# Performance work log

Hardware: AMD Instinct MI355X
Metric: run time of the kernel (lower is better)

## Reference

```python
import jax, jax.numpy as jnp
import numpy as np

B, HD, NQ, NC, NH, NL, NP, NLAY, DFF = 8, 256, 300, 80, 8, 3, 4, 6, 1024
SHAPES = [(80, 80), (40, 40), (20, 20)]
FEAT_CH = [512, 1024, 2048]
DH = HD // NH
EPS_ANCHOR = 0.01


def _linear(x, w, b):
    return x @ w.T + b


def _ln(x, g, b):
    m = x.mean(-1, keepdims=True)
    v = ((x - m) ** 2).mean(-1, keepdims=True)
    return (x - m) / jnp.sqrt(v + 1e-5) * g + b


def _mlp3(x, w1, b1, w2, b2, w3, b3):
    x = jax.nn.relu(_linear(x, w1, b1))
    x = jax.nn.relu(_linear(x, w2, b2))
    return _linear(x, w3, b3)


def _inv_sigmoid(x, eps=1e-5):
    x = jnp.clip(x, 0.0, 1.0)
    return jnp.log(jnp.clip(x, eps, None) / jnp.clip(1.0 - x, eps, None))


def _anchors():
    parts = []
    for lvl, (h, w) in enumerate(SHAPES):
        gy, gx = jnp.meshgrid(jnp.arange(h, dtype=jnp.float32), jnp.arange(w, dtype=jnp.float32), indexing='ij')
        xy = jnp.stack([(gx + 0.5) / w, (gy + 0.5) / h], -1).reshape(-1, 2)
        wh = jnp.full_like(xy, 0.05 * (2.0 ** lvl))
        parts.append(jnp.concatenate([xy, wh], -1))
    a = jnp.concatenate(parts, 0)[None]  # [1, L, 4]
    valid = jnp.all((a > EPS_ANCHOR) & (a < 1 - EPS_ANCHOR), -1, keepdims=True)
    a = jnp.log(a / (1 - a))
    a = jnp.where(valid, a, jnp.float32(1e6))  # finite sentinel for torch's inf
    return a, valid.astype(jnp.float32)


def _mha(q_in, k_in, v_in, wqkv, bqkv, wo, bo):
    wq, wk, wv = jnp.split(wqkv, 3, 0)
    bq, bk, bv = jnp.split(bqkv, 3, 0)
    q = _linear(q_in, wq, bq)
    k = _linear(k_in, wk, bk)
    v = _linear(v_in, wv, bv)
    Bq = q.shape[0]
    sp = lambda t: t.reshape(Bq, -1, NH, DH).transpose(0, 2, 1, 3)
    q, k, v = sp(q), sp(k), sp(v)
    att = jax.nn.softmax(jnp.einsum('bhqd,bhkd->bhqk', q, k) * (1.0 / np.sqrt(DH)), -1)
    out = jnp.einsum('bhqk,bhkd->bhqd', att, v).transpose(0, 2, 1, 3).reshape(Bq, -1, HD)
    return _linear(out, wo, bo)


def _msda(value, loc, aw):
    # value [B,Len,NH,DH], loc [B,Q,NH,NL,NP,2] in [0,1], aw [B,Q,NH,NL,NP]
    Bq, Q = loc.shape[0], loc.shape[1]
    out = jnp.zeros((Bq, Q, NH, DH), value.dtype)
    start = 0
    for lvl, (h, w) in enumerate(SHAPES):
        v = value[:, start:start + h * w]  # [B,hw,NH,DH]
        start += h * w
        # grid_sample align_corners=False pixel coords
        x = loc[..., lvl, :, 0] * w - 0.5  # [B,Q,NH,NP]
        y = loc[..., lvl, :, 1] * h - 0.5
        x0 = jnp.floor(x)
        y0 = jnp.floor(y)
        lx = x - x0
        ly = y - y0
        acc = jnp.zeros((Bq, Q, NH, NP, DH), value.dtype)
        for dy, dx, wt in ((0, 0, (1 - lx) * (1 - ly)), (0, 1, lx * (1 - ly)), (1, 0, (1 - lx) * ly), (1, 1, lx * ly)):
            xi = x0 + dx
            yi = y0 + dy
            ok = ((xi >= 0) & (xi < w) & (yi >= 0) & (yi < h)).astype(value.dtype)  # zero padding
            idx = (jnp.clip(yi, 0, h - 1) * w + jnp.clip(xi, 0, w - 1)).astype(jnp.int32)
            idxf = idx.transpose(0, 1, 3, 2).reshape(Bq, Q * NP, NH)
            g = jnp.take_along_axis(v, idxf[..., None], axis=1)  # [B,Q*NP,NH,DH]
            g = g.reshape(Bq, Q, NP, NH, DH).transpose(0, 1, 3, 2, 4)
            acc = acc + g * (wt * ok)[..., None]
        out = out + (acc * aw[..., lvl, :, None]).sum(3)
    return out.reshape(Bq, Q, HD)


def reference(feat0, feat1, feat2, pw0, bg0, bb0, pw1, bg1, bb1, pw2, bg2, bb2,
              eo_w, eo_b, eln_g, eln_b, es_w, es_b,
              eb_w1, eb_b1, eb_w2, eb_b2, eb_w3, eb_b3,
              qp_w1, qp_b1, qp_w2, qp_b2,
              d_qkv_w, d_qkv_b, d_ao_w, d_ao_b, d_ln1_g, d_ln1_b,
              d_off_w, d_off_b, d_aw_w, d_aw_b, d_val_w, d_val_b,
              d_out_w, d_out_b, d_ln2_g, d_ln2_b,
              d_f1_w, d_f1_b, d_f2_w, d_f2_b, d_ln3_g, d_ln3_b,
              d_sc_w, d_sc_b, d_bb_w1, d_bb_b1, d_bb_w2, d_bb_b2, d_bb_w3, d_bb_b3):
    feats = [feat0, feat1, feat2]
    pws, bgs, bbs = [pw0, pw1, pw2], [bg0, bg1, bg2], [bb0, bb1, bb2]
    toks = []
    for f, pw, g, b in zip(feats, pws, bgs, bbs):
        # 1x1 conv (no bias) + BatchNorm eval (running mean 0, var 1 -> affine)
        t = jnp.einsum('bchw,oc->bhwo', f, pw) * g + b
        toks.append(t.reshape(f.shape[0], -1, HD))
    memory = jnp.concatenate(toks, 1)  # [B, 8400, 256]
    anchors, valid = _anchors()
    memory = memory * valid
    out_mem = _ln(_linear(memory, eo_w, eo_b), eln_g, eln_b)
    scores = _linear(out_mem, es_w, es_b)  # [B,L,NC]
    _, topi = jax.lax.top_k(scores.max(-1), NQ)  # 'default' query select
    gather = lambda t: jnp.take_along_axis(t, topi[..., None], axis=1)
    sel_mem = gather(out_mem)
    anc_b = jnp.broadcast_to(anchors, (memory.shape[0],) + anchors.shape[1:])
    ref_unact = _mlp3(sel_mem, eb_w1, eb_b1, eb_w2, eb_b2, eb_w3, eb_b3) + gather(anc_b)
    tgt = jax.lax.stop_gradient(sel_mem)
    ref = jax.nn.sigmoid(jax.lax.stop_gradient(ref_unact))  # [B,NQ,4]
    Bq = memory.shape[0]
    for i in range(NLAY):
        qpos = _linear(jax.nn.relu(_linear(ref, qp_w1, qp_b1)), qp_w2, qp_b2)
        q = tgt + qpos
        a = _mha(q, q, tgt, d_qkv_w[i], d_qkv_b[i], d_ao_w[i], d_ao_b[i])
        tgt = _ln(tgt + a, d_ln1_g[i], d_ln1_b[i])
        qc = tgt + qpos
        off = _linear(qc, d_off_w[i], d_off_b[i]).reshape(Bq, NQ, NH, NL, NP, 2)
        aw = jax.nn.softmax(_linear(qc, d_aw_w[i], d_aw_b[i]).reshape(Bq, NQ, NH, NL * NP), -1)
        aw = aw.reshape(Bq, NQ, NH, NL, NP)
        r = ref[:, :, None, None, None, :]
        loc = r[..., :2] + off / NP * r[..., 2:] * 0.5
        val = _linear(memory, d_val_w[i], d_val_b[i]).reshape(Bq, -1, NH, DH)
        ca = _linear(_msda(val, loc, aw), d_out_w[i], d_out_b[i])
        tgt = _ln(tgt + ca, d_ln2_g[i], d_ln2_b[i])
        f = _linear(jax.nn.relu(_linear(tgt, d_f1_w[i], d_f1_b[i])), d_f2_w[i], d_f2_b[i])
        tgt = _ln(tgt + f, d_ln3_g[i], d_ln3_b[i])
        delta = _mlp3(tgt, d_bb_w1[i], d_bb_b1[i], d_bb_w2[i], d_bb_b2[i], d_bb_w3[i], d_bb_b3[i])
        new_ref = jax.nn.sigmoid(delta + _inv_sigmoid(ref))
        ref = jax.lax.stop_gradient(new_ref) if i < NLAY - 1 else new_ref
    logits = _linear(tgt, d_sc_w[-1], d_sc_b[-1])
    return jnp.concatenate([logits, ref], -1)  # [B, NQ, NC+4]


def setup_inputs():
    key = jax.random.key(0)
    ks = iter(jax.random.split(key, 80))
    def rn(shape, s=0.02):
        return jax.random.normal(next(ks), shape, jnp.float32) * s
    inp = {}
    for i, (c, (h, w)) in enumerate(zip(FEAT_CH, SHAPES)):
        inp['feat%d' % i] = rn((B, c, h, w), 1.0)
        inp['pw%d' % i] = rn((HD, c), (2.0 / c) ** 0.5)
        inp['bg%d' % i] = jnp.ones((HD,), jnp.float32)
        inp['bb%d' % i] = jnp.zeros((HD,), jnp.float32)
    inp['eo_w'] = rn((HD, HD)); inp['eo_b'] = jnp.zeros((HD,), jnp.float32)
    inp['eln_g'] = jnp.ones((HD,), jnp.float32); inp['eln_b'] = jnp.zeros((HD,), jnp.float32)
    inp['es_w'] = rn((NC, HD)); inp['es_b'] = jnp.zeros((NC,), jnp.float32)
    inp['eb_w1'] = rn((HD, HD)); inp['eb_b1'] = jnp.zeros((HD,), jnp.float32)
    inp['eb_w2'] = rn((HD, HD)); inp['eb_b2'] = jnp.zeros((HD,), jnp.float32)
    inp['eb_w3'] = rn((4, HD)); inp['eb_b3'] = jnp.zeros((4,), jnp.float32)
    inp['qp_w1'] = rn((2 * HD, 4)); inp['qp_b1'] = jnp.zeros((2 * HD,), jnp.float32)
    inp['qp_w2'] = rn((HD, 2 * HD)); inp['qp_b2'] = jnp.zeros((HD,), jnp.float32)
    L = NLAY
    inp['d_qkv_w'] = rn((L, 3 * HD, HD)); inp['d_qkv_b'] = jnp.zeros((L, 3 * HD), jnp.float32)
    inp['d_ao_w'] = rn((L, HD, HD)); inp['d_ao_b'] = jnp.zeros((L, HD), jnp.float32)
    inp['d_ln1_g'] = jnp.ones((L, HD), jnp.float32); inp['d_ln1_b'] = jnp.zeros((L, HD), jnp.float32)
    inp['d_off_w'] = rn((L, NH * NL * NP * 2, HD), 0.005); inp['d_off_b'] = rn((L, NH * NL * NP * 2), 0.1)
    inp['d_aw_w'] = rn((L, NH * NL * NP, HD)); inp['d_aw_b'] = jnp.zeros((L, NH * NL * NP), jnp.float32)
    inp['d_val_w'] = rn((L, HD, HD)); inp['d_val_b'] = jnp.zeros((L, HD), jnp.float32)
    inp['d_out_w'] = rn((L, HD, HD)); inp['d_out_b'] = jnp.zeros((L, HD), jnp.float32)
    inp['d_ln2_g'] = jnp.ones((L, HD), jnp.float32); inp['d_ln2_b'] = jnp.zeros((L, HD), jnp.float32)
    inp['d_f1_w'] = rn((L, DFF, HD)); inp['d_f1_b'] = jnp.zeros((L, DFF), jnp.float32)
    inp['d_f2_w'] = rn((L, HD, DFF)); inp['d_f2_b'] = jnp.zeros((L, HD), jnp.float32)
    inp['d_ln3_g'] = jnp.ones((L, HD), jnp.float32); inp['d_ln3_b'] = jnp.zeros((L, HD), jnp.float32)
    inp['d_sc_w'] = rn((L, NC, HD)); inp['d_sc_b'] = jnp.zeros((L, NC), jnp.float32)
    inp['d_bb_w1'] = rn((L, HD, HD)); inp['d_bb_b1'] = jnp.zeros((L, HD), jnp.float32)
    inp['d_bb_w2'] = rn((L, HD, HD)); inp['d_bb_b2'] = jnp.zeros((L, HD), jnp.float32)
    inp['d_bb_w3'] = rn((L, 4, HD)); inp['d_bb_b3'] = jnp.zeros((L, 4), jnp.float32)
    return inp
```

## Files before the change

kernel.cpp:

```cpp
#include <hip/hip_runtime.h>

constexpr int Bb  = 8;
constexpr int HDn = 256;
constexpr int NQn = 300;
constexpr int NCn = 80;
constexpr int NHn = 8;
constexpr int NPn = 4;
constexpr int Sn  = 8400;
constexpr int MQ  = Bb * NQn;
constexpr int MS  = Bb * Sn;

typedef __attribute__((ext_vector_type(8))) short short8;
typedef __attribute__((ext_vector_type(4))) float floatx4;

__device__ __forceinline__ unsigned short f2bf(float f) {
    unsigned u = __float_as_uint(f);
    unsigned r = u + 0x7FFFu + ((u >> 16) & 1u);
    return (unsigned short)(r >> 16);
}
__device__ __forceinline__ unsigned pack2(float a, float b) {
    return (unsigned)f2bf(a) | ((unsigned)f2bf(b) << 16);
}

__global__ __launch_bounds__(256) void proj_kernel(
    const float* __restrict__ feat, const float* __restrict__ pw,
    const float* __restrict__ bg, const float* __restrict__ bb,
    float* __restrict__ mem,
    int C, int HW, int Wdim, int base)
{
    const int b = blockIdx.z;
    const float* Afeat = feat + (size_t)b * C * HW;
    __shared__ float As[16][128];
    __shared__ float Ws[16][64];
    const int tid = threadIdx.x;
    const int tx = tid & 15, ty = tid >> 4;
    const int p0 = blockIdx.x * 128, o0 = blockIdx.y * 64;
    const int pp4 = (tid & 31) * 4;
    const int cb = tid >> 5;
    const int wrow = tid & 63, wk = (tid >> 6) * 4;
    float acc[8][4] = {};
    for (int k0 = 0; k0 < C; k0 += 16) {
        float4 va0 = make_float4(0.f,0.f,0.f,0.f), va1 = va0;
        if (p0 + pp4 < HW) {
            va0 = *reinterpret_cast<const float4*>(Afeat + (size_t)(k0 + cb) * HW + p0 + pp4);
            va1 = *reinterpret_cast<const float4*>(Afeat + (size_t)(k0 + cb + 8) * HW + p0 + pp4);
        }
        const float4 vw = *reinterpret_cast<const float4*>(pw + (size_t)(o0 + wrow) * C + k0 + wk);
        __syncthreads();
        As[cb][pp4 + 0] = va0.x; As[cb][pp4 + 1] = va0.y; As[cb][pp4 + 2] = va0.z; As[cb][pp4 + 3] = va0.w;
        As[cb + 8][pp4 + 0] = va1.x; As[cb + 8][pp4 + 1] = va1.y; As[cb + 8][pp4 + 2] = va1.z; As[cb + 8][pp4 + 3] = va1.w;
        Ws[wk + 0][wrow] = vw.x; Ws[wk + 1][wrow] = vw.y; Ws[wk + 2][wrow] = vw.z; Ws[wk + 3][wrow] = vw.w;
        __syncthreads();
#pragma unroll
        for (int k = 0; k < 16; ++k) {
            const float4 a0 = *reinterpret_cast<const float4*>(&As[k][ty * 8]);
            const float4 a1 = *reinterpret_cast<const float4*>(&As[k][ty * 8 + 4]);
            const float4 w4 = *reinterpret_cast<const float4*>(&Ws[k][tx * 4]);
            const float av[8] = {a0.x, a0.y, a0.z, a0.w, a1.x, a1.y, a1.z, a1.w};
            const float wv[4] = {w4.x, w4.y, w4.z, w4.w};
#pragma unroll
            for (int i = 0; i < 8; ++i)
#pragma unroll
                for (int j = 0; j < 4; ++j)
                    acc[i][j] = fmaf(av[i], wv[j], acc[i][j]);
        }
    }
#pragma unroll
    for (int i = 0; i < 8; ++i) {
        const int pp = p0 + ty * 8 + i;
        if (pp >= HW) continue;
        const int yy = pp / Wdim, xx = pp - yy * Wdim;
        const float ax = (xx + 0.5f) / Wdim, ay = (yy + 0.5f) / Wdim;
        const float vm = ((ax > 0.01f) && (ax < 0.99f) && (ay > 0.01f) && (ay < 0.99f)) ? 1.f : 0.f;
#pragma unroll
        for (int j = 0; j < 4; ++j) {
            const int o = o0 + tx * 4 + j;
            mem[((size_t)b * Sn + base + pp) * HDn + o] = (acc[i][j] * bg[o] + bb[o]) * vm;
        }
    }
}

__global__ __launch_bounds__(512) void gemm_eoln(
    const float* __restrict__ A,
    const float* __restrict__ W,
    const float* __restrict__ bias,
    const float* __restrict__ g, const float* __restrict__ bt,
    float* __restrict__ O)
{
    __shared__ float As[16][128];
    __shared__ float Ws[16][256];
    const int tid = threadIdx.x;
    const int tx = tid & 31;
    const int ty = tid >> 5;
    const int m0 = blockIdx.x * 128;
    const int arow = tid >> 2, ak = (tid & 3) * 4;
    const int wrow = tid >> 1, wk = (tid & 1) * 8;
    float acc[8][8] = {};
    for (int k0 = 0; k0 < 256; k0 += 16) {
        const float4 a4 = *reinterpret_cast<const float4*>(A + (size_t)(m0 + arow) * 256 + k0 + ak);
        const float4 w0 = *reinterpret_cast<const float4*>(W + (size_t)wrow * 256 + k0 + wk);
        const float4 w1 = *reinterpret_cast<const float4*>(W + (size_t)wrow * 256 + k0 + wk + 4);
        __syncthreads();
        As[ak + 0][arow] = a4.x; As[ak + 1][arow] = a4.y; As[ak + 2][arow] = a4.z; As[ak + 3][arow] = a4.w;
        Ws[wk + 0][wrow] = w0.x; Ws[wk + 1][wrow] = w0.y; Ws[wk + 2][wrow] = w0.z; Ws[wk + 3][wrow] = w0.w;
        Ws[wk + 4][wrow] = w1.x; Ws[wk + 5][wrow] = w1.y; Ws[wk + 6][wrow] = w1.z; Ws[wk + 7][wrow] = w1.w;
        __syncthreads();
#pragma unroll
        for (int k = 0; k < 16; ++k) {
            const float4 a0 = *reinterpret_cast<const float4*>(&As[k][ty * 8]);
            const float4 a1 = *reinterpret_cast<const float4*>(&As[k][ty * 8 + 4]);
            const float4 wv0 = *reinterpret_cast<const float4*>(&Ws[k][tx * 8]);
            const float4 wv1 = *reinterpret_cast<const float4*>(&Ws[k][tx * 8 + 4]);
            const float av[8] = {a0.x, a0.y, a0.z, a0.w, a1.x, a1.y, a1.z, a1.w};
            const float wv[8] = {wv0.x, wv0.y, wv0.z, wv0.w, wv1.x, wv1.y, wv1.z, wv1.w};
#pragma unroll
            for (int i = 0; i < 8; ++i)
#pragma unroll
                for (int j = 0; j < 8; ++j)
                    acc[i][j] = fmaf(av[i], wv[j], acc[i][j]);
        }
    }
    float bv[8], gv[8], btv[8];
#pragma unroll
    for (int j = 0; j < 8; ++j) {
        bv[j] = bias[tx * 8 + j];
        gv[j] = g[tx * 8 + j];
        btv[j] = bt[tx * 8 + j];
    }
#pragma unroll
    for (int i = 0; i < 8; ++i) {
        float s1 = 0.f, s2 = 0.f;
#pragma unroll
        for (int j = 0; j < 8; ++j) {
            const float v = acc[i][j] + bv[j];
            acc[i][j] = v;
            s1 += v; s2 += v * v;
        }
#pragma unroll
        for (int o = 1; o < 32; o <<= 1) {
            s1 += __shfl_xor(s1, o, 64);
            s2 += __shfl_xor(s2, o, 64);
        }
        const float mean = s1 * (1.f / 256.f);
        const float var  = s2 * (1.f / 256.f) - mean * mean;
        const float inv  = rsqrtf(var + 1e-5f);
        float out[8];
#pragma unroll
        for (int j = 0; j < 8; ++j) out[j] = (acc[i][j] - mean) * inv * gv[j] + btv[j];
        float* op = O + (size_t)(m0 + ty * 8 + i) * 256 + tx * 8;
        *reinterpret_cast<float4*>(op) = make_float4(out[0], out[1], out[2], out[3]);
        *reinterpret_cast<float4*>(op + 4) = make_float4(out[4], out[5], out[6], out[7]);
    }
}

__global__ __launch_bounds__(256) void gemm_es(
    const float* __restrict__ A,
    const float* __restrict__ W,
    const float* __restrict__ bias,
    float* __restrict__ smax)
{
    __shared__ float As[16][64];
    __shared__ float Ws[16][80];
    const int tid = threadIdx.x;
    const int tx = tid & 15;
    const int ty = tid >> 4;
    const int m0 = blockIdx.x * 64;
    const int arow = tid >> 2, ak = (tid & 3) * 4;
    float acc[4][5] = {};
    for (int k0 = 0; k0 < 256; k0 += 16) {
        const float4 a4 = *reinterpret_cast<const float4*>(A + (size_t)(m0 + arow) * 256 + k0 + ak);
        float4 w0 = make_float4(0.f,0.f,0.f,0.f), w1 = w0;
        const int wrow = tid >> 1, wk = (tid & 1) * 8;
        if (tid < 160) {
            w0 = *reinterpret_cast<const float4*>(W + (size_t)wrow * 256 + k0 + wk);
            w1 = *reinterpret_cast<const float4*>(W + (size_t)wrow * 256 + k0 + wk + 4);
        }
        __syncthreads();
        As[ak + 0][arow] = a4.x; As[ak + 1][arow] = a4.y; As[ak + 2][arow] = a4.z; As[ak + 3][arow] = a4.w;
        if (tid < 160) {
            Ws[wk + 0][wrow] = w0.x; Ws[wk + 1][wrow] = w0.y; Ws[wk + 2][wrow] = w0.z; Ws[wk + 3][wrow] = w0.w;
            Ws[wk + 4][wrow] = w1.x; Ws[wk + 5][wrow] = w1.y; Ws[wk + 6][wrow] = w1.z; Ws[wk + 7][wrow] = w1.w;
        }
        __syncthreads();
#pragma unroll
        for (int k = 0; k < 16; ++k) {
            const float4 a4v = *reinterpret_cast<const float4*>(&As[k][ty * 4]);
            const float av[4] = {a4v.x, a4v.y, a4v.z, a4v.w};
            float wv[5];
#pragma unroll
            for (int j = 0; j < 5; ++j) wv[j] = Ws[k][tx * 5 + j];
#pragma unroll
            for (int i = 0; i < 4; ++i)
#pragma unroll
                for (int j = 0; j < 5; ++j)
                    acc[i][j] = fmaf(av[i], wv[j], acc[i][j]);
        }
    }
    float bv[5];
#pragma unroll
    for (int j = 0; j < 5; ++j) bv[j] = bias[tx * 5 + j];
#pragma unroll
    for (int i = 0; i < 4; ++i) {
        float vmax = -3.0e38f;
#pragma unroll
        for (int j = 0; j < 5; ++j) vmax = fmaxf(vmax, acc[i][j] + bv[j]);
#pragma unroll
        for (int o = 1; o < 16; o <<= 1) vmax = fmaxf(vmax, __shfl_xor(vmax, o, 64));
        if (tx == 0) smax[m0 + ty * 4 + i] = vmax;
    }
}

__global__ void fconv_kernel(const float* __restrict__ in, unsigned short* __restrict__ out, int n4)
{
    const int i = blockIdx.x * 256 + threadIdx.x;
    if (i >= n4) return;
    const float4 v = reinterpret_cast<const float4*>(in)[i];
    reinterpret_cast<uint2*>(out)[i] = make_uint2(pack2(v.x, v.y), pack2(v.z, v.w));
}

__global__ __launch_bounds__(512) void gemm_vbig(
    const unsigned short* __restrict__ A,
    const float* __restrict__ W,
    const float* __restrict__ bias,
    unsigned short* __restrict__ C,
    int M)
{
    __shared__ __align__(16) unsigned short As[128 * 40];
    __shared__ __align__(16) unsigned short Bs[256 * 40];
    const int tid = threadIdx.x;
    const int lane = tid & 63, wid = tid >> 6;
    const int wm = wid >> 2, wn = wid & 3;
    const int m0 = blockIdx.x * 128, n0 = blockIdx.y * 256;
    const int arow = tid >> 2, ak = (tid & 3) * 8;
    const int brow = tid >> 1, bk = (tid & 1) * 16;
    const int fs = (lane >> 4) * 8;
    floatx4 acc[4][4];
#pragma unroll
    for (int i = 0; i < 4; ++i)
#pragma unroll
        for (int j = 0; j < 4; ++j) acc[i][j] = (floatx4){0.f, 0.f, 0.f, 0.f};

    for (int k0 = 0; k0 < 256; k0 += 32) {
        const short8 a8 = *reinterpret_cast<const short8*>(A + (size_t)(m0 + arow) * 256 + k0 + ak);
        float wv[16];
        {
            const float* wp = W + (size_t)(n0 + brow) * 256 + k0 + bk;
#pragma unroll
            for (int j = 0; j < 4; ++j) *reinterpret_cast<float4*>(&wv[4 * j]) = *reinterpret_cast<const float4*>(wp + 4 * j);
        }
        __syncthreads();
        *reinterpret_cast<short8*>(&As[arow * 40 + ak]) = a8;
        *reinterpret_cast<uint4*>(&Bs[brow * 40 + bk]) =
            make_uint4(pack2(wv[0], wv[1]), pack2(wv[2], wv[3]), pack2(wv[4], wv[5]), pack2(wv[6], wv[7]));
        *reinterpret_cast<uint4*>(&Bs[brow * 40 + bk + 8]) =
            make_uint4(pack2(wv[8], wv[9]), pack2(wv[10], wv[11]), pack2(wv[12], wv[13]), pack2(wv[14], wv[15]));
        __syncthreads();
        short8 af[4], bf[4];
#pragma unroll
        for (int mi = 0; mi < 4; ++mi)
            af[mi] = *reinterpret_cast<const short8*>(&As[(wm * 64 + mi * 16 + (lane & 15)) * 40 + fs]);
#pragma unroll
        for (int ni = 0; ni < 4; ++ni)
            bf[ni] = *reinterpret_cast<const short8*>(&Bs[(wn * 64 + ni * 16 + (lane & 15)) * 40 + fs]);
#pragma unroll
        for (int mi = 0; mi < 4; ++mi)
#pragma unroll
            for (int ni = 0; ni < 4; ++ni)
                acc[mi][ni] = __builtin_amdgcn_mfma_f32_16x16x32_bf16(af[mi], bf[ni], acc[mi][ni], 0, 0, 0);
    }
#pragma unroll
    for (int mi = 0; mi < 4; ++mi) {
        const int rowb = m0 + wm * 64 + mi * 16 + (lane >> 4) * 4;
#pragma unroll
        for (int ni = 0; ni < 4; ++ni) {
            const int col = n0 + wn * 64 + ni * 16 + (lane & 15);
            const float bv = bias[col];
#pragma unroll
            for (int r = 0; r < 4; ++r)
                C[(size_t)(rowb + r) * 1536 + col] = f2bf(acc[mi][ni][r] + bv);
        }
    }
}

template <int ACT>
__global__ __launch_bounds__(256) void gemm_sm(
    const float* __restrict__ A, const float* __restrict__ A2, int a2_nlim, int lda,
    const float* __restrict__ W, int ldw,
    const float* __restrict__ bias,
    float* __restrict__ C, int ldc,
    int M, int N, int K)
{
    constexpr int LD = 264;
    __shared__ __align__(16) unsigned short As[64 * LD];
    __shared__ __align__(16) unsigned short Bs[64 * LD];
    const int tid = threadIdx.x;
    const int lane = tid & 63, wid = tid >> 6;
    const int wr = wid >> 1, wc = wid & 1;
    const int m0 = blockIdx.x * 64, n0 = blockIdx.y * 64;
    const float* A2e = (A2 && n0 < a2_nlim) ? A2 : nullptr;
    const int srow = tid >> 2;
    const int cb   = (tid & 3) * 16;
    const int fs = (lane >> 4) * 8;
    floatx4 acc[2][2];
#pragma unroll
    for (int i = 0; i < 2; ++i)
#pragma unroll
        for (int j = 0; j < 2; ++j) acc[i][j] = (floatx4){0.f, 0.f, 0.f, 0.f};

    for (int kc = 0; kc < K; kc += 256) {
        if (kc) __syncthreads();
        {
            const bool mok = (m0 + srow < M);
            const float* ap = A + (size_t)(m0 + srow) * lda + kc;
            const float* ap2 = A2e ? A2e + (size_t)(m0 + srow) * lda + kc : nullptr;
#pragma unroll
            for (int c = 0; c < 4; ++c) {
                float4 v[4];
#pragma unroll
                for (int j = 0; j < 4; ++j) {
                    v[j] = make_float4(0.f, 0.f, 0.f, 0.f);
                    if (mok) {
                        v[j] = *reinterpret_cast<const float4*>(ap + cb + c * 64 + j * 4);
                        if (ap2) {
                            const float4 v2 = *reinterpret_cast<const float4*>(ap2 + cb + c * 64 + j * 4);
                            v[j].x += v2.x; v[j].y += v2.y; v[j].z += v2.z; v[j].w += v2.w;
                        }
                    }
                }
#pragma unroll
                for (int j = 0; j < 4; ++j)
                    *reinterpret_cast<uint2*>(&As[srow * LD + cb + c * 64 + j * 4]) =
                        make_uint2(pack2(v[j].x, v[j].y), pack2(v[j].z, v[j].w));
            }
        }
        {
            const bool nok = (n0 + srow < N);
            const float* wp = W + (size_t)(n0 + srow) * ldw + kc;
#pragma unroll
            for (int c = 0; c < 4; ++c) {
                float4 v[4];
#pragma unroll
                for (int j = 0; j < 4; ++j) {
                    v[j] = make_float4(0.f, 0.f, 0.f, 0.f);
                    if (nok) v[j] = *reinterpret_cast<const float4*>(wp + cb + c * 64 + j * 4);
                }
#pragma unroll
                for (int j = 0; j < 4; ++j)
                    *reinterpret_cast<uint2*>(&Bs[srow * LD + cb + c * 64 + j * 4]) =
                        make_uint2(pack2(v[j].x, v[j].y), pack2(v[j].z, v[j].w));
            }
        }
        __syncthreads();
#pragma unroll
        for (int ks = 0; ks < 8; ++ks) {
            short8 af[2], bf[2];
#pragma unroll
            for (int mi = 0; mi < 2; ++mi)
                af[mi] = *reinterpret_cast<const short8*>(&As[(wr * 32 + mi * 16 + (lane & 15)) * LD + ks * 32 + fs]);
#pragma unroll
            for (int ni = 0; ni < 2; ++ni)
                bf[ni] = *reinterpret_cast<const short8*>(&Bs[(wc * 32 + ni * 16 + (lane & 15)) * LD + ks * 32 + fs]);
#pragma unroll
// ... 267 lines not shown
    __shared__ float Om[NQn][32];
    __shared__ float Mm[NQn];
    __shared__ float Lm[NQn];
    const int t = threadIdx.x;
    for (int i = t; i < NQn * 32; i += 640) {
        const int kk = i >> 5, d = i & 31;
        const size_t src = ((size_t)(b * NQn + kk)) * 768 + h * 32 + d;
        Ks[kk][d] = QKV[src + 256];
        Vs[kk][d] = QKV[src + 512];
    }
    __syncthreads();
    const int half = (t >= 320) ? 1 : 0;
    const int q = half ? (t - 320) : t;
    float m = -1e30f, l = 0.f;
    float o[32];
    if (q < NQn) {
        float qv[32];
        const float* qp = QKV + ((size_t)(b * NQn + q)) * 768 + h * 32;
#pragma unroll
        for (int d = 0; d < 32; ++d) qv[d] = qp[d] * 0.17677669529663687f;
#pragma unroll
        for (int d = 0; d < 32; ++d) o[d] = 0.f;
        const int k0 = half * 150, k1 = k0 + 150;
        for (int kk = k0; kk < k1; ++kk) {
            float s0 = 0.f, s1 = 0.f, s2 = 0.f, s3 = 0.f;
#pragma unroll
            for (int d = 0; d < 32; d += 4) {
                s0 = fmaf(qv[d + 0], Ks[kk][d + 0], s0);
                s1 = fmaf(qv[d + 1], Ks[kk][d + 1], s1);
                s2 = fmaf(qv[d + 2], Ks[kk][d + 2], s2);
                s3 = fmaf(qv[d + 3], Ks[kk][d + 3], s3);
            }
            const float s = (s0 + s1) + (s2 + s3);
            if (s > m + 8.f) {
                const float cf = __expf(m - s);
                m = s;
                l *= cf;
#pragma unroll
                for (int d = 0; d < 32; ++d) o[d] *= cf;
            }
            const float pv = __expf(s - m);
            l += pv;
#pragma unroll
            for (int d = 0; d < 32; ++d) o[d] = fmaf(pv, Vs[kk][d], o[d]);
        }
        if (half) {
            Mm[q] = m; Lm[q] = l;
#pragma unroll
            for (int d = 0; d < 32; ++d) Om[q][d] = o[d];
        }
    }
    __syncthreads();
    if (!half && q < NQn) {
        const float m2 = Mm[q], l2 = Lm[q];
        const float mm = fmaxf(m, m2);
        const float c1 = __expf(m - mm), c2 = __expf(m2 - mm);
        const float L = l * c1 + l2 * c2;
        const float inv = 1.f / L;
        float* op = O + ((size_t)(b * NQn + q)) * HDn + h * 32;
#pragma unroll
        for (int d = 0; d < 32; ++d) op[d] = (o[d] * c1 + Om[q][d] * c2) * inv;
    }
}

__global__ void concat_oaw(const float* __restrict__ offw, const float* __restrict__ offbias,
                           const float* __restrict__ aww, const float* __restrict__ awbias,
                           float* __restrict__ cw, float* __restrict__ cb)
{
    const int idx = blockIdx.x * 256 + threadIdx.x;
    const int TW = 6 * 288 * 256;
    if (idx < TW) {
        const int i = idx / (288 * 256);
        const int r = (idx / 256) % 288;
        const int c = idx & 255;
        cw[idx] = (r < 192) ? offw[((size_t)i * 192 + r) * 256 + c]
                            : aww[((size_t)i * 96 + (r - 192)) * 256 + c];
    } else if (idx < TW + 6 * 288) {
        const int j = idx - TW;
        const int i = j / 288, r = j % 288;
        cb[j] = (r < 192) ? offbias[i * 192 + r] : awbias[i * 96 + (r - 192)];
    }
}

__global__ void softmax12_kernel(float* __restrict__ oaw)
{
    const int g = blockIdx.x * 256 + threadIdx.x;
    if (g >= MQ * NHn) return;
    float* p = oaw + (size_t)(g >> 3) * 288 + 192 + (g & 7) * 12;
    float mx = -1e30f;
#pragma unroll
    for (int i = 0; i < 12; ++i) mx = fmaxf(mx, p[i]);
    float e[12];
    float s = 0.f;
#pragma unroll
    for (int i = 0; i < 12; ++i) { e[i] = expf(p[i] - mx); s += e[i]; }
    const float inv = 1.f / s;
#pragma unroll
    for (int i = 0; i < 12; ++i) p[i] = e[i] * inv;
}

__global__ __launch_bounds__(256) void msda_kernel(const unsigned short* __restrict__ val, int ldv,
                                                   const float* __restrict__ oaw,
                                                   const float* __restrict__ ref,
                                                   float* __restrict__ out)
{
    const int mq = blockIdx.x;
    const int b = mq / NQn;
    const int t = threadIdx.x;
    const int h = t >> 5, d = t & 31;
    __shared__ float s_ref[4];
    __shared__ float s_aw[96];
    __shared__ float s_off[192];
    if (t < 4) s_ref[t] = ref[mq * 4 + t];
    if (t < 96) s_aw[t] = oaw[(size_t)mq * 288 + 192 + t];
    if (t < 192) s_off[t] = oaw[(size_t)mq * 288 + t];
    __syncthreads();
    const int Wl[3] = {80, 40, 20};
    const int base[3] = {0, 6400, 8000};
    float acc = 0.f;
#pragma unroll
    for (int l = 0; l < 3; ++l) {
        const int W = Wl[l];
        const unsigned short* vb = val + ((size_t)b * Sn + base[l]) * ldv + h * 32 + d;
#pragma unroll
        for (int p = 0; p < 4; ++p) {
            const float ox = s_off[((h * 3 + l) * 4 + p) * 2 + 0];
            const float oy = s_off[((h * 3 + l) * 4 + p) * 2 + 1];
            const float locx = s_ref[0] + ox * (1.f / NPn) * s_ref[2] * 0.5f;
            const float locy = s_ref[1] + oy * (1.f / NPn) * s_ref[3] * 0.5f;
            const float x = locx * W - 0.5f;
            const float y = locy * W - 0.5f;
            const float x0f = floorf(x), y0f = floorf(y);
            const float lx = x - x0f, ly = y - y0f;
            const int x0 = (int)x0f, y0 = (int)y0f;
            const float a = s_aw[h * 12 + l * 4 + p];
            const float wts[4] = {(1.f - lx) * (1.f - ly), lx * (1.f - ly), (1.f - lx) * ly, lx * ly};
            float sum = 0.f;
#pragma unroll
            for (int c2 = 0; c2 < 4; ++c2) {
                const int xi = x0 + (c2 & 1);
                const int yi = y0 + (c2 >> 1);
                const bool ok = (xi >= 0) && (xi < W) && (yi >= 0) && (yi < W);
                const int xc = min(max(xi, 0), W - 1);
                const int yc = min(max(yi, 0), W - 1);
                const float v = __uint_as_float((unsigned)vb[(size_t)(yc * W + xc) * ldv] << 16);
                sum = fmaf(wts[c2], ok ? v : 0.f, sum);
            }
            acc = fmaf(a, sum, acc);
        }
    }
    out[(size_t)mq * HDn + t] = acc;
}

__global__ void copy_ref_kernel(const float* __restrict__ ref, float* __restrict__ out)
{
    const int m = blockIdx.x * 256 + threadIdx.x;
    if (m >= MQ) return;
#pragma unroll
    for (int c = 0; c < 4; ++c) out[(size_t)m * 84 + 80 + c] = ref[m * 4 + c];
}

extern "C" void kernel_launch(void* const* d_in, const int* in_sizes, int n_in,
                              void* d_out, int out_size, void* d_ws, size_t ws_size,
                              hipStream_t stream)
{
    (void)in_sizes; (void)n_in; (void)out_size;
    const float* feat0 = (const float*)d_in[0];
    const float* pw0   = (const float*)d_in[1];
    const float* bg0   = (const float*)d_in[2];
    const float* bb0   = (const float*)d_in[3];
    const float* feat1 = (const float*)d_in[4];
    const float* pw1   = (const float*)d_in[5];
    const float* bg1   = (const float*)d_in[6];
    const float* bb1   = (const float*)d_in[7];
    const float* feat2 = (const float*)d_in[8];
    const float* pw2   = (const float*)d_in[9];
    const float* bg2   = (const float*)d_in[10];
    const float* bb2   = (const float*)d_in[11];
    const float* eo_w  = (const float*)d_in[12];
    const float* eo_b  = (const float*)d_in[13];
    const float* eln_g = (const float*)d_in[14];
    const float* eln_b = (const float*)d_in[15];
    const float* es_w  = (const float*)d_in[16];
    const float* es_b  = (const float*)d_in[17];
    const float* eb_w1 = (const float*)d_in[18];
    const float* eb_b1 = (const float*)d_in[19];
    const float* eb_w2 = (const float*)d_in[20];
    const float* eb_b2 = (const float*)d_in[21];
    const float* eb_w3 = (const float*)d_in[22];
    const float* eb_b3 = (const float*)d_in[23];
    const float* qp_w1 = (const float*)d_in[24];
    const float* qp_b1 = (const float*)d_in[25];
    const float* qp_w2 = (const float*)d_in[26];
    const float* qp_b2 = (const float*)d_in[27];
    const float* d_qkv_w = (const float*)d_in[28];
    const float* d_qkv_b = (const float*)d_in[29];
    const float* d_ao_w  = (const float*)d_in[30];
    const float* d_ao_b  = (const float*)d_in[31];
    const float* d_ln1_g = (const float*)d_in[32];
    const float* d_ln1_b = (const float*)d_in[33];
    const float* d_off_w = (const float*)d_in[34];
    const float* d_off_b = (const float*)d_in[35];
    const float* d_aw_w  = (const float*)d_in[36];
    const float* d_aw_b  = (const float*)d_in[37];
    const float* d_val_w = (const float*)d_in[38];
    const float* d_val_b = (const float*)d_in[39];
    const float* d_out_w = (const float*)d_in[40];
    const float* d_out_b = (const float*)d_in[41];
    const float* d_ln2_g = (const float*)d_in[42];
    const float* d_ln2_b = (const float*)d_in[43];
    const float* d_f1_w  = (const float*)d_in[44];
    const float* d_f1_b  = (const float*)d_in[45];
    const float* d_f2_w  = (const float*)d_in[46];
    const float* d_f2_b  = (const float*)d_in[47];
    const float* d_ln3_g = (const float*)d_in[48];
    const float* d_ln3_b = (const float*)d_in[49];
    const float* d_sc_w  = (const float*)d_in[50];
    const float* d_sc_b  = (const float*)d_in[51];
    const float* d_bb_w1 = (const float*)d_in[52];
    const float* d_bb_b1 = (const float*)d_in[53];
    const float* d_bb_w2 = (const float*)d_in[54];
    const float* d_bb_b2 = (const float*)d_in[55];
    const float* d_bb_w3 = (const float*)d_in[56];
    const float* d_bb_b3 = (const float*)d_in[57];

    float* ws = (float*)d_ws;
    size_t off = 0;
    auto alloc = [&](size_t n) { float* p = ws + off; off += (n + 63) & ~(size_t)63; return p; };
    float* memory = alloc((size_t)MS * HDn);
    float* om     = alloc((size_t)MS * HDn);
    float* smaxb  = alloc((size_t)MS);
    int*   topi   = (int*)alloc((size_t)MQ);
    float* tgt    = alloc((size_t)MQ * HDn);
    float* refb   = alloc((size_t)MQ * 4);
    float* qpos   = alloc((size_t)MQ * HDn);
    float* qkvb   = alloc((size_t)MQ * 768);
    float* atto   = alloc((size_t)MQ * HDn);
    float* abuf   = alloc((size_t)MQ * HDn);
    float* oawb   = alloc((size_t)MQ * 288);
    float* msd    = alloc((size_t)MQ * HDn);
    float* ffb    = alloc((size_t)MQ * 1024);
    float* qb     = alloc((size_t)MQ * HDn);
    float* kb     = alloc((size_t)MQ * HDn);
    float* cw     = alloc((size_t)6 * 288 * 256);
    float* cb     = alloc((size_t)6 * 288);
    const size_t VALBIG_FLOATS = (size_t)MS * 768;
    unsigned short* valbig = nullptr;
    if ((off + VALBIG_FLOATS + 64) * sizeof(float) <= ws_size)
        valbig = (unsigned short*)alloc(VALBIG_FLOATS);
    const bool batched = (valbig != nullptr);
    unsigned short* ombf = (unsigned short*)om;
    float* outp = (float*)d_out;

    concat_oaw<<<(6 * 288 * 256 + 6 * 288 + 255) / 256, 256, 0, stream>>>(d_off_w, d_off_b, d_aw_w, d_aw_b, cw, cb);

    proj_kernel<<<dim3(50, 4, 8), 256, 0, stream>>>(feat0, pw0, bg0, bb0, memory, 512, 6400, 80, 0);
    proj_kernel<<<dim3(13, 4, 8), 256, 0, stream>>>(feat1, pw1, bg1, bb1, memory, 1024, 1600, 40, 6400);
    proj_kernel<<<dim3(4, 4, 8), 256, 0, stream>>>(feat2, pw2, bg2, bb2, memory, 2048, 400, 20, 8000);

    gemm_eoln<<<525, 512, 0, stream>>>(memory, eo_w, eo_b, eln_g, eln_b, om);
    gemm_es<<<1050, 256, 0, stream>>>(om, es_w, es_b, smaxb);
    topk_kernel<<<Bb, 256, 0, stream>>>(smaxb, topi);
    gather_kernel<<<MQ, 256, 0, stream>>>(om, topi, tgt);

    gemm_sm<1><<<dim3(38, 4), 256, 0, stream>>>(tgt, nullptr, 0, HDn, eb_w1, HDn, eb_b1, qb, HDn, MQ, HDn, HDn);
    gemm_sm<1><<<dim3(38, 4), 256, 0, stream>>>(qb, nullptr, 0, HDn, eb_w2, HDn, eb_b2, kb, HDn, MQ, HDn, HDn);
    head4_kernel<0><<<600, 256, 0, stream>>>(kb, eb_w3, eb_b3, topi, refb);

    if (batched) {
        fconv_kernel<<<(MS * HDn / 4 + 255) / 256, 256, 0, stream>>>(memory, ombf, MS * HDn / 4);
        gemm_vbig<<<dim3(525, 6), 512, 0, stream>>>(ombf, d_val_w, d_val_b, valbig, MS);
    }

    for (int i = 0; i < 6; ++i) {
        const float* wqkv = d_qkv_w + (size_t)i * 768 * 256;
        const float* bqkv = d_qkv_b + (size_t)i * 768;
        gemm_qpos<<<dim3(19, 2), 256, 0, stream>>>(refb, qp_w1, qp_b1, qp_w2, qp_b2, qpos, MQ);
        gemm_sm<0><<<dim3(38, 12), 256, 0, stream>>>(tgt, qpos, 512, HDn, wqkv, HDn, bqkv, qkvb, 768, MQ, 768, HDn);
        mha_kernel<<<dim3(NHn, Bb), 640, 0, stream>>>(qkvb, atto);
        gemm_sm<0><<<dim3(38, 4), 256, 0, stream>>>(atto, nullptr, 0, HDn, d_ao_w + (size_t)i * 65536, HDn,
                                                    d_ao_b + (size_t)i * 256, abuf, HDn, MQ, HDn, HDn);
        ln_kernel<<<MQ, 256, 0, stream>>>(abuf, tgt, d_ln1_g + (size_t)i * 256, d_ln1_b + (size_t)i * 256, tgt);
        gemm_sm<0><<<dim3(38, 5), 256, 0, stream>>>(tgt, qpos, 1 << 30, HDn, cw + (size_t)i * 288 * 256, HDn,
                                                    cb + (size_t)i * 288, oawb, 288, MQ, 288, HDn);
        softmax12_kernel<<<(MQ * NHn + 255) / 256, 256, 0, stream>>>(oawb);
        const unsigned short* valptr;
        int ldv;
        if (batched) { valptr = valbig + (size_t)i * 256; ldv = 1536; }
        else {
            fconv_kernel<<<(MS * HDn / 4 + 255) / 256, 256, 0, stream>>>(memory, (unsigned short*)ffb, MS * HDn / 4);
            gemm_vbig<<<dim3(525, 1), 512, 0, stream>>>((unsigned short*)ffb, d_val_w + (size_t)i * 65536,
                                                        d_val_b + (size_t)i * 256, ombf, MS);
            valptr = ombf; ldv = 1536;
        }
        msda_kernel<<<MQ, 256, 0, stream>>>(valptr, ldv, oawb, refb, msd);
        gemm_sm<0><<<dim3(38, 4), 256, 0, stream>>>(msd, nullptr, 0, HDn, d_out_w + (size_t)i * 65536, HDn,
                                                    d_out_b + (size_t)i * 256, abuf, HDn, MQ, HDn, HDn);
        ln_kernel<<<MQ, 256, 0, stream>>>(abuf, tgt, d_ln2_g + (size_t)i * 256, d_ln2_b + (size_t)i * 256, tgt);
        gemm_sm<1><<<dim3(38, 16), 256, 0, stream>>>(tgt, nullptr, 0, HDn, d_f1_w + (size_t)i * 1024 * 256, HDn,
                                                     d_f1_b + (size_t)i * 1024, ffb, 1024, MQ, 1024, HDn);
        gemm_sm<0><<<dim3(38, 4), 256, 0, stream>>>(ffb, nullptr, 0, 1024, d_f2_w + (size_t)i * 256 * 1024, 1024,
                                                    d_f2_b + (size_t)i * 256, abuf, HDn, MQ, HDn, 1024);
        ln_kernel<<<MQ, 256, 0, stream>>>(abuf, tgt, d_ln3_g + (size_t)i * 256, d_ln3_b + (size_t)i * 256, tgt);
        gemm_sm<1><<<dim3(38, 4), 256, 0, stream>>>(tgt, nullptr, 0, HDn, d_bb_w1 + (size_t)i * 65536, HDn,
                                                    d_bb_b1 + (size_t)i * 256, qb, HDn, MQ, HDn, HDn);
        gemm_sm<1><<<dim3(38, 4), 256, 0, stream>>>(qb, nullptr, 0, HDn, d_bb_w2 + (size_t)i * 65536, HDn,
                                                    d_bb_b2 + (size_t)i * 256, kb, HDn, MQ, HDn, HDn);
        head4_kernel<1><<<600, 256, 0, stream>>>(kb, d_bb_w3 + (size_t)i * 1024, d_bb_b3 + (size_t)i * 4, nullptr, refb);
    }

    gemm_sm<0><<<dim3(38, 2), 256, 0, stream>>>(tgt, nullptr, 0, HDn, d_sc_w + (size_t)5 * 80 * 256, HDn,
                                                d_sc_b + (size_t)5 * 80, outp, 84, MQ, NCn, HDn);
    copy_ref_kernel<<<(MQ + 255) / 256, 256, 0, stream>>>(refb, outp);
}
```

Baseline: 2.587 ms.

## Fuse fp32-to-bf16 conversion into value GEMM and double proj k-tile

```diff
diff --git a/kernel.cpp b/kernel.cpp
--- a/kernel.cpp
+++ b/kernel.cpp
@@ -30,8 +30,8 @@
 {
     const int b = blockIdx.z;
     const float* Afeat = feat + (size_t)b * C * HW;
-    __shared__ float As[16][128];
-    __shared__ float Ws[16][64];
+    __shared__ float As[32][128];
+    __shared__ float Ws[32][64];
     const int tid = threadIdx.x;
     const int tx = tid & 15, ty = tid >> 4;
     const int p0 = blockIdx.x * 128, o0 = blockIdx.y * 64;
@@ -39,20 +39,29 @@
     const int cb = tid >> 5;
     const int wrow = tid & 63, wk = (tid >> 6) * 4;
     float acc[8][4] = {};
-    for (int k0 = 0; k0 < C; k0 += 16) {
-        float4 va0 = make_float4(0.f,0.f,0.f,0.f), va1 = va0;
-        if (p0 + pp4 < HW) {
-            va0 = *reinterpret_cast<const float4*>(Afeat + (size_t)(k0 + cb) * HW + p0 + pp4);
-            va1 = *reinterpret_cast<const float4*>(Afeat + (size_t)(k0 + cb + 8) * HW + p0 + pp4);
-        }
-        const float4 vw = *reinterpret_cast<const float4*>(pw + (size_t)(o0 + wrow) * C + k0 + wk);
-        __syncthreads();
-        As[cb][pp4 + 0] = va0.x; As[cb][pp4 + 1] = va0.y; As[cb][pp4 + 2] = va0.z; As[cb][pp4 + 3] = va0.w;
-        As[cb + 8][pp4 + 0] = va1.x; As[cb + 8][pp4 + 1] = va1.y; As[cb + 8][pp4 + 2] = va1.z; As[cb + 8][pp4 + 3] = va1.w;
-        Ws[wk + 0][wrow] = vw.x; Ws[wk + 1][wrow] = vw.y; Ws[wk + 2][wrow] = vw.z; Ws[wk + 3][wrow] = vw.w;
-        __syncthreads();
-#pragma unroll
-        for (int k = 0; k < 16; ++k) {
+    for (int k0 = 0; k0 < C; k0 += 32) {
+        float4 va[4];
+#pragma unroll
+        for (int c4 = 0; c4 < 4; ++c4) {
+            va[c4] = make_float4(0.f, 0.f, 0.f, 0.f);
+            if (p0 + pp4 < HW)
+                va[c4] = *reinterpret_cast<const float4*>(Afeat + (size_t)(k0 + cb + 8 * c4) * HW + p0 + pp4);
+        }
+        const float4 vw0 = *reinterpret_cast<const float4*>(pw + (size_t)(o0 + wrow) * C + k0 + wk);
+        const float4 vw1 = *reinterpret_cast<const float4*>(pw + (size_t)(o0 + wrow) * C + k0 + wk + 16);
+        __syncthreads();
+#pragma unroll
+        for (int c4 = 0; c4 < 4; ++c4) {
+            As[cb + 8 * c4][pp4 + 0] = va[c4].x;
+            As[cb + 8 * c4][pp4 + 1] = va[c4].y;
+            As[cb + 8 * c4][pp4 + 2] = va[c4].z;
+            As[cb + 8 * c4][pp4 + 3] = va[c4].w;
+        }
+        Ws[wk + 0][wrow] = vw0.x; Ws[wk + 1][wrow] = vw0.y; Ws[wk + 2][wrow] = vw0.z; Ws[wk + 3][wrow] = vw0.w;
+        Ws[wk + 16][wrow] = vw1.x; Ws[wk + 17][wrow] = vw1.y; Ws[wk + 18][wrow] = vw1.z; Ws[wk + 19][wrow] = vw1.w;
+        __syncthreads();
+#pragma unroll
+        for (int k = 0; k < 32; ++k) {
             const float4 a0 = *reinterpret_cast<const float4*>(&As[k][ty * 8]);
             const float4 a1 = *reinterpret_cast<const float4*>(&As[k][ty * 8 + 4]);
             const float4 w4 = *reinterpret_cast<const float4*>(&Ws[k][tx * 4]);
@@ -210,74 +219,85 @@
     }
 }
 
-__global__ void fconv_kernel(const float* __restrict__ in, unsigned short* __restrict__ out, int n4)
-{
-    const int i = blockIdx.x * 256 + threadIdx.x;
-    if (i >= n4) return;
-    const float4 v = reinterpret_cast<const float4*>(in)[i];
-    reinterpret_cast<uint2*>(out)[i] = make_uint2(pack2(v.x, v.y), pack2(v.z, v.w));
-}
-
-__global__ __launch_bounds__(512) void gemm_vbig(
-    const unsigned short* __restrict__ A,
+__global__ __launch_bounds__(512) void gemm_vbig2(
+    const float* __restrict__ A,
     const float* __restrict__ W,
     const float* __restrict__ bias,
     unsigned short* __restrict__ C,
-    int M)
-{
-    __shared__ __align__(16) unsigned short As[128 * 40];
+    int ldc, int NT, int M)
+{
+    __shared__ __align__(16) unsigned short Af[128 * 264];
     __shared__ __align__(16) unsigned short Bs[256 * 40];
     const int tid = threadIdx.x;
     const int lane = tid & 63, wid = tid >> 6;
     const int wm = wid >> 2, wn = wid & 3;
-    const int m0 = blockIdx.x * 128, n0 = blockIdx.y * 256;
-    const int arow = tid >> 2, ak = (tid & 3) * 8;
+    const int m0 = blockIdx.x * 128;
+    const int fs = (lane >> 4) * 8;
+    {
+        const int arow = tid >> 2, ac = (tid & 3) * 16;
+        const float* ap = A + (size_t)(m0 + arow) * 256;
+#pragma unroll
+        for (int c4 = 0; c4 < 4; ++c4) {
+            const int col = ac + c4 * 64;
+            float v[16];
+#pragma unroll
+            for (int j = 0; j < 4; ++j)
+                *reinterpret_cast<float4*>(&v[4 * j]) = *reinterpret_cast<const float4*>(ap + col + 4 * j);
+            *reinterpret_cast<uint4*>(&Af[arow * 264 + col]) =
+                make_uint4(pack2(v[0], v[1]), pack2(v[2], v[3]), pack2(v[4], v[5]), pack2(v[6], v[7]));
+            *reinterpret_cast<uint4*>(&Af[arow * 264 + col + 8]) =
+                make_uint4(pack2(v[8], v[9]), pack2(v[10], v[11]), pack2(v[12], v[13]), pack2(v[14], v[15]));
+        }
+    }
+    __syncthreads();
     const int brow = tid >> 1, bk = (tid & 1) * 16;
-    const int fs = (lane >> 4) * 8;
-    floatx4 acc[4][4];
-#pragma unroll
-    for (int i = 0; i < 4; ++i)
-#pragma unroll
-        for (int j = 0; j < 4; ++j) acc[i][j] = (floatx4){0.f, 0.f, 0.f, 0.f};
-
-    for (int k0 = 0; k0 < 256; k0 += 32) {
-        const short8 a8 = *reinterpret_cast<const short8*>(A + (size_t)(m0 + arow) * 256 + k0 + ak);
-        float wv[16];
-        {
-            const float* wp = W + (size_t)(n0 + brow) * 256 + k0 + bk;
-#pragma unroll
-            for (int j = 0; j < 4; ++j) *reinterpret_cast<float4*>(&wv[4 * j]) = *reinterpret_cast<const float4*>(wp + 4 * j);
-        }
-        __syncthreads();
-        *reinterpret_cast<short8*>(&As[arow * 40 + ak]) = a8;
-        *reinterpret_cast<uint4*>(&Bs[brow * 40 + bk]) =
-            make_uint4(pack2(wv[0], wv[1]), pack2(wv[2], wv[3]), pack2(wv[4], wv[5]), pack2(wv[6], wv[7]));
-        *reinterpret_cast<uint4*>(&Bs[brow * 40 + bk + 8]) =
-            make_uint4(pack2(wv[8], wv[9]), pack2(wv[10], wv[11]), pack2(wv[12], wv[13]), pack2(wv[14], wv[15]));
-        __syncthreads();
-        short8 af[4], bf[4];
-#pragma unroll
-        for (int mi = 0; mi < 4; ++mi)
-            af[mi] = *reinterpret_cast<const short8*>(&As[(wm * 64 + mi * 16 + (lane & 15)) * 40 + fs]);
-#pragma unroll
-        for (int ni = 0; ni < 4; ++ni)
-            bf[ni] = *reinterpret_cast<const short8*>(&Bs[(wn * 64 + ni * 16 + (lane & 15)) * 40 + fs]);
-#pragma unroll
-        for (int mi = 0; mi < 4; ++mi)
+    for (int nt = 0; nt < NT; ++nt) {
+        const int n0 = nt * 256;
+        floatx4 acc[4][4];
+#pragma unroll
+        for (int i = 0; i < 4; ++i)
+#pragma unroll
+            for (int j = 0; j < 4; ++j) acc[i][j] = (floatx4){0.f, 0.f, 0.f, 0.f};
+        for (int kc = 0; kc < 256; kc += 32) {
+            if (nt || kc) __syncthreads();
+            {
+                const float* wp = W + (size_t)(n0 + brow) * 256 + kc + bk;
+                float v[16];
+#pragma unroll
+                for (int j = 0; j < 4; ++j)
+                    *reinterpret_cast<float4*>(&v[4 * j]) = *reinterpret_cast<const float4*>(wp + 4 * j);
+                *reinterpret_cast<uint4*>(&Bs[brow * 40 + bk]) =
+                    make_uint4(pack2(v[0], v[1]), pack2(v[2], v[3]), pack2(v[4], v[5]), pack2(v[6], v[7]));
+                *reinterpret_cast<uint4*>(&Bs[brow * 40 + bk + 8]) =
+                    make_uint4(pack2(v[8], v[9]), pack2(v[10], v[11]), pack2(v[12], v[13]), pack2(v[14], v[15]));
+            }
+            __syncthreads();
+            short8 af[4], bf[4];
+#pragma unroll
+            for (int mi = 0; mi < 4; ++mi)
+                af[mi] = *reinterpret_cast<const short8*>(&Af[(wm * 64 + mi * 16 + (lane & 15)) * 264 + kc + fs]);
 #pragma unroll
             for (int ni = 0; ni < 4; ++ni)
-                acc[mi][ni] = __builtin_amdgcn_mfma_f32_16x16x32_bf16(af[mi], bf[ni], acc[mi][ni], 0, 0, 0);
-    }
-#pragma unroll
-    for (int mi = 0; mi < 4; ++mi) {
-        const int rowb = m0 + wm * 64 + mi * 16 + (lane >> 4) * 4;
-#pragma unroll
-        for (int ni = 0; ni < 4; ++ni) {
-            const int col = n0 + wn * 64 + ni * 16 + (lane & 15);
-            const float bv = bias[col];
-#pragma unroll
-            for (int r = 0; r < 4; ++r)
-                C[(size_t)(rowb + r) * 1536 + col] = f2bf(acc[mi][ni][r] + bv);
+                bf[ni] = *reinterpret_cast<const short8*>(&Bs[(wn * 64 + ni * 16 + (lane & 15)) * 40 + fs]);
+#pragma unroll
+            for (int mi = 0; mi < 4; ++mi)
+#pragma unroll
+                for (int ni = 0; ni < 4; ++ni)
+                    acc[mi][ni] = __builtin_amdgcn_mfma_f32_16x16x32_bf16(af[mi], bf[ni], acc[mi][ni], 0, 0, 0);
+        }
+#pragma unroll
+        for (int mi = 0; mi < 4; ++mi) {
+            const int rowb = m0 + wm * 64 + mi * 16 + (lane >> 4) * 4;
+#pragma unroll
+            for (int ni = 0; ni < 4; ++ni) {
+                const int col = n0 + wn * 64 + ni * 16 + (lane & 15);
+                const float bv = bias[col];
+#pragma unroll
+                for (int r = 0; r < 4; ++r) {
+                    const int row = rowb + r;
+                    if (row < M) C[(size_t)row * ldc + col] = f2bf(acc[mi][ni][r] + bv);
+                }
+            }
         }
     }
 }
@@ -896,10 +916,8 @@
     gemm_sm<1><<<dim3(38, 4), 256, 0, stream>>>(qb, nullptr, 0, HDn, eb_w2, HDn, eb_b2, kb, HDn, MQ, HDn, HDn);
     head4_kernel<0><<<600, 256, 0, stream>>>(kb, eb_w3, eb_b3, topi, refb);
 
-    if (batched) {
-        fconv_kernel<<<(MS * HDn / 4 + 255) / 256, 256, 0, stream>>>(memory, ombf, MS * HDn / 4);
-        gemm_vbig<<<dim3(525, 6), 512, 0, stream>>>(ombf, d_val_w, d_val_b, valbig, MS);
-    }
+    if (batched)
+        gemm_vbig2<<<525, 512, 0, stream>>>(memory, d_val_w, d_val_b, valbig, 1536, 6, MS);
 
     for (int i = 0; i < 6; ++i) {
         const float* wqkv = d_qkv_w + (size_t)i * 768 * 256;
@@ -917,10 +935,9 @@
         int ldv;
         if (batched) { valptr = valbig + (size_t)i * 256; ldv = 1536; }
         else {
-            fconv_kernel<<<(MS * HDn / 4 + 255) / 256, 256, 0, stream>>>(memory, (unsigned short*)ffb, MS * HDn / 4);
-            gemm_vbig<<<dim3(525, 1), 512, 0, stream>>>((unsigned short*)ffb, d_val_w + (size_t)i * 65536,
-                                                        d_val_b + (size_t)i * 256, ombf, MS);
-            valptr = ombf; ldv = 1536;
+            gemm_vbig2<<<525, 512, 0, stream>>>(memory, d_val_w + (size_t)i * 65536,
+                                                d_val_b + (size_t)i * 256, ombf, 256, 1, MS);
+            valptr = ombf; ldv = 256;
         }
         msda_kernel<<<MQ, 256, 0, stream>>>(valptr, ldv, oawb, refb, msd);
         gemm_sm<0><<<dim3(38, 4), 256, 0, stream>>>(msd, nullptr, 0, HDn, d_out_w + (size_t)i * 65536, HDn,
```

New measurement: 2.708 ms. +4.7%, slower.

## Fuse attention-weight softmax into MSDA, widen proj K-tile, add ldc to value GEMM

Applied to the files above, without the earlier changes.

```diff
diff --git a/kernel.cpp b/kernel.cpp
--- a/kernel.cpp
+++ b/kernel.cpp
@@ -30,8 +30,8 @@
 {
     const int b = blockIdx.z;
     const float* Afeat = feat + (size_t)b * C * HW;
-    __shared__ float As[16][128];
-    __shared__ float Ws[16][64];
+    __shared__ float As[32][128];
+    __shared__ float Ws[32][64];
     const int tid = threadIdx.x;
     const int tx = tid & 15, ty = tid >> 4;
     const int p0 = blockIdx.x * 128, o0 = blockIdx.y * 64;
@@ -39,20 +39,29 @@
     const int cb = tid >> 5;
     const int wrow = tid & 63, wk = (tid >> 6) * 4;
     float acc[8][4] = {};
-    for (int k0 = 0; k0 < C; k0 += 16) {
-        float4 va0 = make_float4(0.f,0.f,0.f,0.f), va1 = va0;
-        if (p0 + pp4 < HW) {
-            va0 = *reinterpret_cast<const float4*>(Afeat + (size_t)(k0 + cb) * HW + p0 + pp4);
-            va1 = *reinterpret_cast<const float4*>(Afeat + (size_t)(k0 + cb + 8) * HW + p0 + pp4);
-        }
-        const float4 vw = *reinterpret_cast<const float4*>(pw + (size_t)(o0 + wrow) * C + k0 + wk);
-        __syncthreads();
-        As[cb][pp4 + 0] = va0.x; As[cb][pp4 + 1] = va0.y; As[cb][pp4 + 2] = va0.z; As[cb][pp4 + 3] = va0.w;
-        As[cb + 8][pp4 + 0] = va1.x; As[cb + 8][pp4 + 1] = va1.y; As[cb + 8][pp4 + 2] = va1.z; As[cb + 8][pp4 + 3] = va1.w;
-        Ws[wk + 0][wrow] = vw.x; Ws[wk + 1][wrow] = vw.y; Ws[wk + 2][wrow] = vw.z; Ws[wk + 3][wrow] = vw.w;
-        __syncthreads();
-#pragma unroll
-        for (int k = 0; k < 16; ++k) {
+    for (int k0 = 0; k0 < C; k0 += 32) {
+        float4 va[4];
+#pragma unroll
+        for (int c4 = 0; c4 < 4; ++c4) {
+            va[c4] = make_float4(0.f, 0.f, 0.f, 0.f);
+            if (p0 + pp4 < HW)
+                va[c4] = *reinterpret_cast<const float4*>(Afeat + (size_t)(k0 + cb + 8 * c4) * HW + p0 + pp4);
+        }
+        const float4 vw0 = *reinterpret_cast<const float4*>(pw + (size_t)(o0 + wrow) * C + k0 + wk);
+        const float4 vw1 = *reinterpret_cast<const float4*>(pw + (size_t)(o0 + wrow) * C + k0 + wk + 16);
+        __syncthreads();
+#pragma unroll
+        for (int c4 = 0; c4 < 4; ++c4) {
+            As[cb + 8 * c4][pp4 + 0] = va[c4].x;
+            As[cb + 8 * c4][pp4 + 1] = va[c4].y;
+            As[cb + 8 * c4][pp4 + 2] = va[c4].z;
+            As[cb + 8 * c4][pp4 + 3] = va[c4].w;
+        }
+        Ws[wk + 0][wrow] = vw0.x; Ws[wk + 1][wrow] = vw0.y; Ws[wk + 2][wrow] = vw0.z; Ws[wk + 3][wrow] = vw0.w;
+        Ws[wk + 16][wrow] = vw1.x; Ws[wk + 17][wrow] = vw1.y; Ws[wk + 18][wrow] = vw1.z; Ws[wk + 19][wrow] = vw1.w;
+        __syncthreads();
+#pragma unroll
+        for (int k = 0; k < 32; ++k) {
             const float4 a0 = *reinterpret_cast<const float4*>(&As[k][ty * 8]);
             const float4 a1 = *reinterpret_cast<const float4*>(&As[k][ty * 8 + 4]);
             const float4 w4 = *reinterpret_cast<const float4*>(&Ws[k][tx * 4]);
@@ -222,7 +231,7 @@
     const unsigned short* __restrict__ A,
     const float* __restrict__ W,
     const float* __restrict__ bias,
-    unsigned short* __restrict__ C,
+    unsigned short* __restrict__ C, int ldc,
     int M)
 {
     __shared__ __align__(16) unsigned short As[128 * 40];
@@ -277,7 +286,7 @@
             const float bv = bias[col];
 #pragma unroll
             for (int r = 0; r < 4; ++r)
-                C[(size_t)(rowb + r) * 1536 + col] = f2bf(acc[mi][ni][r] + bv);
+                C[(size_t)(rowb + r) * ldc + col] = f2bf(acc[mi][ni][r] + bv);
         }
     }
 }
@@ -711,23 +720,6 @@
     }
 }
 
-__global__ void softmax12_kernel(float* __restrict__ oaw)
-{
-    const int g = blockIdx.x * 256 + threadIdx.x;
-    if (g >= MQ * NHn) return;
-    float* p = oaw + (size_t)(g >> 3) * 288 + 192 + (g & 7) * 12;
-    float mx = -1e30f;
-#pragma unroll
-    for (int i = 0; i < 12; ++i) mx = fmaxf(mx, p[i]);
-    float e[12];
-    float s = 0.f;
-#pragma unroll
-    for (int i = 0; i < 12; ++i) { e[i] = expf(p[i] - mx); s += e[i]; }
-    const float inv = 1.f / s;
-#pragma unroll
-    for (int i = 0; i < 12; ++i) p[i] = e[i] * inv;
-}
-
 __global__ __launch_bounds__(256) void msda_kernel(const unsigned short* __restrict__ val, int ldv,
                                                    const float* __restrict__ oaw,
                                                    const float* __restrict__ ref,
@@ -743,6 +735,20 @@
     if (t < 4) s_ref[t] = ref[mq * 4 + t];
     if (t < 96) s_aw[t] = oaw[(size_t)mq * 288 + 192 + t];
     if (t < 192) s_off[t] = oaw[(size_t)mq * 288 + t];
+    __syncthreads();
+    if (t < 8) {
+        float* p = s_aw + t * 12;
+        float mx = -1e30f;
+#pragma unroll
+        for (int i = 0; i < 12; ++i) mx = fmaxf(mx, p[i]);
+        float e[12];
+        float s = 0.f;
+#pragma unroll
+        for (int i = 0; i < 12; ++i) { e[i] = expf(p[i] - mx); s += e[i]; }
+        const float inv = 1.f / s;
+#pragma unroll
+        for (int i = 0; i < 12; ++i) p[i] = e[i] * inv;
+    }
     __syncthreads();
     const int Wl[3] = {80, 40, 20};
     const int base[3] = {0, 6400, 8000};
@@ -898,7 +904,7 @@
 
     if (batched) {
         fconv_kernel<<<(MS * HDn / 4 + 255) / 256, 256, 0, stream>>>(memory, ombf, MS * HDn / 4);
-        gemm_vbig<<<dim3(525, 6), 512, 0, stream>>>(ombf, d_val_w, d_val_b, valbig, MS);
+        gemm_vbig<<<dim3(525, 6), 512, 0, stream>>>(ombf, d_val_w, d_val_b, valbig, 1536, MS);
     }
 
     for (int i = 0; i < 6; ++i) {
@@ -912,15 +918,14 @@
         ln_kernel<<<MQ, 256, 0, stream>>>(abuf, tgt, d_ln1_g + (size_t)i * 256, d_ln1_b + (size_t)i * 256, tgt);
         gemm_sm<0><<<dim3(38, 5), 256, 0, stream>>>(tgt, qpos, 1 << 30, HDn, cw + (size_t)i * 288 * 256, HDn,
                                                     cb + (size_t)i * 288, oawb, 288, MQ, 288, HDn);
-        softmax12_kernel<<<(MQ * NHn + 255) / 256, 256, 0, stream>>>(oawb);
         const unsigned short* valptr;
         int ldv;
         if (batched) { valptr = valbig + (size_t)i * 256; ldv = 1536; }
         else {
             fconv_kernel<<<(MS * HDn / 4 + 255) / 256, 256, 0, stream>>>(memory, (unsigned short*)ffb, MS * HDn / 4);
             gemm_vbig<<<dim3(525, 1), 512, 0, stream>>>((unsigned short*)ffb, d_val_w + (size_t)i * 65536,
-                                                        d_val_b + (size_t)i * 256, ombf, MS);
-            valptr = ombf; ldv = 1536;
+                                                        d_val_b + (size_t)i * 256, ombf, 256, MS);
+            valptr = ombf; ldv = 256;
         }
         msda_kernel<<<MQ, 256, 0, stream>>>(valptr, ldv, oawb, refb, msd);
         gemm_sm<0><<<dim3(38, 4), 256, 0, stream>>>(msd, nullptr, 0, HDn, d_out_w + (size_t)i * 65536, HDn,
```

Result: faster. 2.524 ms (-2.4%).
